# Kernel optimization log

Hardware: AMD Instinct MI355X
Metric: run time of the kernel (lower is better)

The kernel has to match this reference:

```python
import jax, jax.numpy as jnp
import numpy as np

B, H, S, D = 4, 16, 1024, 64
MAX_REL = 16  # max_relative_position


def setup_inputs() -> dict:
    key = jax.random.key(0)
    kq, kk, kv, kr = jax.random.split(key, 4)
    Q = jax.random.normal(kq, (B, H, S, D), dtype=jnp.float32)
    K = jax.random.normal(kk, (B, H, S, D), dtype=jnp.float32)
    V = jax.random.normal(kv, (B, H, S, D), dtype=jnp.float32)
    # learned relative-position embedding table [2*P+1, d_k]
    rel_table = jax.random.normal(kr, (2 * MAX_REL + 1, D), dtype=jnp.float32) * 0.02
    # causal mask, broadcastable over batch/heads; 0 => masked
    mask = jnp.tril(jnp.ones((S, S), dtype=jnp.int32))[None, None, :, :]
    return {"Q": Q, "K": K, "V": V, "rel_table": rel_table, "mask": mask}


def reference(Q, K, V, rel_table, mask):
    scale = jnp.sqrt(jnp.asarray(Q.shape[-1], Q.dtype))
    seq_len = Q.shape[2]
    r = jnp.arange(seq_len)
    # clipped relative distances -> embedding indices in [0, 2P]
    idx = jnp.clip(r[None, :] - r[:, None], -MAX_REL, MAX_REL) + MAX_REL  # [S,S]
    rel_emb = rel_table[idx]  # [S, S, D]
    scores = jnp.einsum('bhld,bhrd->bhlr', Q, K) / scale  # [B,H,S,S]
    scores = scores + jnp.einsum('bhld,lrd->bhlr', Q, rel_emb)
    scores = jnp.where(mask == 0, -jnp.inf, scores)
    attn = jax.nn.softmax(scores, axis=-1)
    output = jnp.einsum('bhlr,bhrd->bhld', attn, V)  # [B,H,S,D]
    return (output, attn)
```

## Files before the change

### kernel.cpp

```cpp
#include <hip/hip_runtime.h>

#define S_ 1024
#define D_ 64
#define RT 16
#define SCP 1036

typedef _Float16 f16x4 __attribute__((ext_vector_type(4)));
typedef _Float16 f16x8 __attribute__((ext_vector_type(8)));
typedef __fp16  h16x2 __attribute__((ext_vector_type(2)));
typedef float f32x4 __attribute__((ext_vector_type(4)));

__global__ __launch_bounds__(256)
void prep_kv(const float* __restrict__ K, const float* __restrict__ V,
             _Float16* __restrict__ Kws, _Float16* __restrict__ VT) {
    if (blockIdx.x < 1024) {
        const int idx = blockIdx.x * 256 + threadIdx.x;
        const int g4  = idx & 3;
        const float* kp = K + (size_t)(idx >> 2) * 64 + g4 * 16;
        _Float16* dst = Kws + (size_t)(idx >> 2) * 64 + g4 * 16;
        f16x8 o0, o1;
        #pragma unroll
        for (int u = 0; u < 2; ++u) {
            float4 f0 = *reinterpret_cast<const float4*>(kp + 8 * u);
            float4 f1 = *reinterpret_cast<const float4*>(kp + 8 * u + 4);
            f16x8& o = u ? o1 : o0;
            o[0] = (_Float16)f0.x; o[1] = (_Float16)f0.y;
            o[2] = (_Float16)f0.z; o[3] = (_Float16)f0.w;
            o[4] = (_Float16)f1.x; o[5] = (_Float16)f1.y;
            o[6] = (_Float16)f1.z; o[7] = (_Float16)f1.w;
        }
        *reinterpret_cast<f16x8*>(dst)     = o0;
        *reinterpret_cast<f16x8*>(dst + 8) = o1;
    } else {
        const int idx = (blockIdx.x - 1024) * 256 + threadIdx.x;
        const int bh  = idx >> 12;
        const int kt  = (idx >> 6) & 63;
        const int col = idx & 63;
        const float* vp = V + ((size_t)bh * S_ + kt * 16) * D_ + col;
        _Float16* dst = VT + ((size_t)(bh * 64 + kt) * 64 + col) * 16;
        f16x8 a, b;
        #pragma unroll
        for (int kk = 0; kk < 16; ++kk) {
            float f = vp[(size_t)kk * D_];
            if (kk < 8) a[kk] = (_Float16)f; else b[kk - 8] = (_Float16)f;
        }
        *reinterpret_cast<f16x8*>(dst)     = a;
        *reinterpret_cast<f16x8*>(dst + 8) = b;
    }
}

__global__ __launch_bounds__(256, 4)
void relattn_main(const float* __restrict__ Q, const float* __restrict__ rel,
                  const _Float16* __restrict__ Kws, const _Float16* __restrict__ VT,
                  float* __restrict__ outO, float* outA) {
    __shared__ __align__(16) _Float16 sc[RT * SCP];
    __shared__ float qrel[RT * 17];
    __shared__ float rowsum[4][RT];

    const int tid  = threadIdx.x;
    const int lane = tid & 63;
    const int w    = tid >> 6;
    const int l15  = lane & 15;
    const int g4   = lane >> 4;
    const int bid  = blockIdx.x;
    const int bh   = (bid & 7) + 8 * (bid >> 9);
    const int tile = 63 - ((bid >> 3) & 63);
    const int R0   = tile * RT;
    const int nt16 = tile + 1;

    const float* Qb = Q + (size_t)bh * S_ * D_;
    const _Float16* Kb = Kws + (size_t)bh * 64 * 1024;
    const _Float16* Vt = VT  + (size_t)bh * 64 * 1024;

    {
        const int z0 = 16 * nt16;
        const f16x8 zz = {0, 0, 0, 0, 0, 0, 0, 0};
        const int i = tid >> 4;
        for (int c = z0 + (tid & 15) * 8; c < S_; c += 128)
            *reinterpret_cast<f16x8*>(&sc[i * SCP + c]) = zz;
    }

    {
        int idx = tid;
        #pragma unroll
        for (int rep = 0; rep < 2; ++rep) {
            if (idx < RT * 17) {
                const int i = idx / 17;
                const int j = idx - i * 17;
                const float* qp = Qb + (size_t)(R0 + i) * D_;
                const float* rp = rel + j * D_;
                float s = 0.f;
                #pragma unroll
                for (int d = 0; d < D_; d += 4) {
                    float4 a = *reinterpret_cast<const float4*>(qp + d);
                    float4 b = *reinterpret_cast<const float4*>(rp + d);
                    s += a.x * b.x + a.y * b.y + a.z * b.z + a.w * b.w;
                }
                qrel[idx] = s;
            }
            idx = 256 + tid;
        }
    }

    f16x8 aq0, aq1;
    {
        const float* qp = Qb + (size_t)(R0 + l15) * D_ + 8 * g4;
        float4 f0 = *reinterpret_cast<const float4*>(qp);
        float4 f1 = *reinterpret_cast<const float4*>(qp + 4);
        float4 f2 = *reinterpret_cast<const float4*>(qp + 32);
        float4 f3 = *reinterpret_cast<const float4*>(qp + 36);
        aq0 = f16x8{(_Float16)(f0.x*0.125f), (_Float16)(f0.y*0.125f),
                    (_Float16)(f0.z*0.125f), (_Float16)(f0.w*0.125f),
                    (_Float16)(f1.x*0.125f), (_Float16)(f1.y*0.125f),
                    (_Float16)(f1.z*0.125f), (_Float16)(f1.w*0.125f)};
        aq1 = f16x8{(_Float16)(f2.x*0.125f), (_Float16)(f2.y*0.125f),
                    (_Float16)(f2.z*0.125f), (_Float16)(f2.w*0.125f),
                    (_Float16)(f3.x*0.125f), (_Float16)(f3.y*0.125f),
                    (_Float16)(f3.z*0.125f), (_Float16)(f3.w*0.125f)};
    }

    __syncthreads();

    const int   myrow = R0 + l15;
    const float qr0v  = qrel[l15 * 17];
    const int fastmax = (R0 - 31) >> 4;

    float psum = 0.f;
    auto qk_load = [&](int ct, f16x8* kf) {
        const _Float16* kp = Kb + ((size_t)ct * 16 + l15) * 64 + 8 * g4;
        kf[0] = *reinterpret_cast<const f16x8*>(kp);
        kf[1] = *reinterpret_cast<const f16x8*>(kp + 32);
    };
    auto qk_compute = [&](int ct, const f16x8* kf) {
        f32x4 acc = {0.f, 0.f, 0.f, 0.f};
        acc = __builtin_amdgcn_mfma_f32_16x16x32_f16(kf[0], aq0, acc, 0, 0, 0);
        acc = __builtin_amdgcn_mfma_f32_16x16x32_f16(kf[1], aq1, acc, 0, 0, 0);
        float e[4];
        if (ct <= fastmax) {
            #pragma unroll
            for (int j = 0; j < 4; ++j) e[j] = __expf(acc[j] + qr0v);
        } else {
            #pragma unroll
            for (int j = 0; j < 4; ++j) {
                const int dlt = myrow - (ct * 16 + 4 * g4 + j);
                e[j] = 0.f;
                if (dlt >= 0)
                    e[j] = __expf(acc[j] + ((dlt < 16) ? qrel[l15 * 17 + 16 - dlt]
                                                       : qr0v));
            }
        }
        psum += (e[0] + e[1]) + (e[2] + e[3]);
        h16x2 lo = __builtin_amdgcn_cvt_pkrtz(e[0], e[1]);
        h16x2 hi = __builtin_amdgcn_cvt_pkrtz(e[2], e[3]);
        f16x4 pk = {(_Float16)lo[0], (_Float16)lo[1],
                    (_Float16)hi[0], (_Float16)hi[1]};
        *reinterpret_cast<f16x4*>(&sc[l15 * SCP + ct * 16 + 4 * g4]) = pk;
    };

    for (int ct0 = w; ct0 < nt16; ct0 += 16) {
        f16x8 k0[2], k1[2], k2[2], k3[2];
        const bool h1 = (ct0 + 4)  < nt16;
        const bool h2 = (ct0 + 8)  < nt16;
        const bool h3 = (ct0 + 12) < nt16;
        qk_load(ct0, k0);
        if (h1) qk_load(ct0 + 4,  k1);
        if (h2) qk_load(ct0 + 8,  k2);
        if (h3) qk_load(ct0 + 12, k3);
        qk_compute(ct0, k0);
        if (h1) qk_compute(ct0 + 4,  k1);
        if (h2) qk_compute(ct0 + 8,  k2);
        if (h3) qk_compute(ct0 + 12, k3);
    }

    const int n0    = 16 * w;
    const int ktile = nt16;
    const int fg    = ktile >> 2;
    const int tail  = ktile & 3;
    const _Float16* vtb = Vt + ((size_t)(n0 + l15)) * 16 + 4 * g4;

    f16x4 bvA[4], bvB[4], bvC[4];
    auto pv_load = [&](int g, f16x4* bv) {
        #pragma unroll
        for (int u = 0; u < 4; ++u)
            bv[u] = *reinterpret_cast<const f16x4*>(vtb + (size_t)(4 * g + u) * 1024);
    };
    if (fg > 0) pv_load(0, bvA);
    if (fg > 1) pv_load(1, bvB);

    psum += __shfl_xor(psum, 16);
    psum += __shfl_xor(psum, 32);
    if (lane < 16) rowsum[w][lane] = psum;
    __syncthreads();

    f32x4 oa[4] = {{0,0,0,0},{0,0,0,0},{0,0,0,0},{0,0,0,0}};
    auto pv_mfma = [&](int g, const f16x4* bv) {
        #pragma unroll
        for (int u = 0; u < 4; ++u) {
            f16x4 ap = *reinterpret_cast<f16x4*>(
                &sc[l15 * SCP + (4 * g + u) * 16 + 4 * g4]);
            oa[u] = __builtin_amdgcn_mfma_f32_16x16x16f16(ap, bv[u], oa[u], 0, 0, 0);
        }
    };

    float* Ab = outA + ((size_t)bh * S_ + R0) * S_;
    #pragma unroll
    for (int ii = 0; ii < 4; ++ii) {
        const int i = 4 * w + ii;
        const float iv = 1.f / (rowsum[0][i] + rowsum[1][i] +
                                rowsum[2][i] + rowsum[3][i]);
        #pragma unroll
        for (int q = 0; q < 4; ++q) {
            const int c = q * 256 + lane * 4;
            f16x4 sv = *reinterpret_cast<f16x4*>(&sc[i * SCP + c]);
            f32x4 o = {(float)sv[0] * iv, (float)sv[1] * iv,
                       (float)sv[2] * iv, (float)sv[3] * iv};
            __builtin_nontemporal_store(
                o, reinterpret_cast<f32x4*>(Ab + (size_t)i * S_ + c));
        }
    }

    if (fg > 2) pv_load(2, bvC);
    int g = 0;
    for (; g + 3 < fg; g += 3) {
        pv_mfma(g, bvA);
        pv_load(g + 3, bvA);
        pv_mfma(g + 1, bvB);
        if (g + 4 < fg) pv_load(g + 4, bvB);
        pv_mfma(g + 2, bvC);
        if (g + 5 < fg) pv_load(g + 5, bvC);
    }
    if (g < fg)     pv_mfma(g, bvA);
    if (g + 1 < fg) pv_mfma(g + 1, bvB);
    if (g + 2 < fg) pv_mfma(g + 2, bvC);

    for (int r = 0; r < tail; ++r) {
        const int kt = 4 * fg + r;
        f16x4 bv = *reinterpret_cast<const f16x4*>(vtb + (size_t)kt * 1024);
        f16x4 ap = *reinterpret_cast<f16x4*>(&sc[l15 * SCP + kt * 16 + 4 * g4]);
        oa[r] = __builtin_amdgcn_mfma_f32_16x16x16f16(ap, bv, oa[r], 0, 0, 0);
    }

    f32x4 op = (oa[0] + oa[1]) + (oa[2] + oa[3]);

    float* Ob = outO + (size_t)bh * S_ * D_;
    #pragma unroll
    for (int j = 0; j < 4; ++j) {
        const int row = 4 * g4 + j;
        const float s = rowsum[0][row] + rowsum[1][row] +
                        rowsum[2][row] + rowsum[3][row];
        Ob[(size_t)(R0 + row) * D_ + n0 + l15] = op[j] / s;
    }
}

extern "C" void kernel_launch(void* const* d_in, const int* in_sizes, int n_in,
                              void* d_out, int out_size, void* d_ws, size_t ws_size,
                              hipStream_t stream) {
    const float* Q   = (const float*)d_in[0];
    const float* K   = (const float*)d_in[1];
    const float* V   = (const float*)d_in[2];
    const float* rel = (const float*)d_in[3];

    float* out  = (float*)d_out;
    float* outO = out;
    float* outA = out + (size_t)4 * 16 * 1024 * 64;

    _Float16*  Kws  = (_Float16*)((char*)d_ws + (size_t)(1 << 20));
    _Float16*  VTws = (_Float16*)((char*)d_ws + (size_t)(10 << 20));

    prep_kv<<<dim3(2048), dim3(256), 0, stream>>>(K, V, Kws, VTws);
    relattn_main<<<dim3(4096), dim3(256), 0, stream>>>(Q, rel, Kws, VTws,
                                                       outO, outA);
}
```

Before: 122.1 us.

## Double-buffer K fragment loads and trim zero-fill of score tile

The QK loop is restructured to double-buffer K fragments (kA/kB), prefetching the next group of four column tiles while computing the current one. The first K loads are issued before the block barrier so they overlap the qrel setup. The shared-memory zero fill now only covers up to the next 256-column boundary, and fully masked 256-column chunks of the attention output are written as zeros without reading shared memory. In exchange it holds 16 f16x8 buffers in registers, which may pressure occupancy under launch_bounds(256,4).

```diff
diff --git a/kernel.cpp b/kernel.cpp
--- a/kernel.cpp
+++ b/kernel.cpp
@@ -67,17 +67,18 @@
     const int tile = 63 - ((bid >> 3) & 63);
     const int R0   = tile * RT;
     const int nt16 = tile + 1;
+    const int bound = 16 * nt16;
 
     const float* Qb = Q + (size_t)bh * S_ * D_;
     const _Float16* Kb = Kws + (size_t)bh * 64 * 1024;
     const _Float16* Vt = VT  + (size_t)bh * 64 * 1024;
 
     {
-        const int z0 = 16 * nt16;
+        const int mend = (bound + 255) & ~255;
         const f16x8 zz = {0, 0, 0, 0, 0, 0, 0, 0};
-        const int i = tid >> 4;
-        for (int c = z0 + (tid & 15) * 8; c < S_; c += 128)
-            *reinterpret_cast<f16x8*>(&sc[i * SCP + c]) = zz;
+        const int r = tid >> 4;
+        for (int c = bound + (tid & 15) * 8; c < mend; c += 128)
+            *reinterpret_cast<f16x8*>(&sc[r * SCP + c]) = zz;
     }
 
     {
@@ -119,8 +120,6 @@
                     (_Float16)(f3.z*0.125f), (_Float16)(f3.w*0.125f)};
     }
 
-    __syncthreads();
-
     const int   myrow = R0 + l15;
     const float qr0v  = qrel[l15 * 17];
     const int fastmax = (R0 - 31) >> 4;
@@ -131,6 +130,20 @@
         kf[0] = *reinterpret_cast<const f16x8*>(kp);
         kf[1] = *reinterpret_cast<const f16x8*>(kp + 32);
     };
+    auto qk_load4 = [&](int ct0, f16x8* buf) {
+        #pragma unroll
+        for (int u = 0; u < 4; ++u)
+            if (ct0 + 4 * u < nt16) qk_load(ct0 + 4 * u, buf + 2 * u);
+    };
+
+    f16x8 kA[8], kB[8];
+    qk_load4(w, kA);
+
+    __syncthreads();
+
+    const float qr0 = qrel[l15 * 17];
+    (void)qr0v;
+
     auto qk_compute = [&](int ct, const f16x8* kf) {
         f32x4 acc = {0.f, 0.f, 0.f, 0.f};
         acc = __builtin_amdgcn_mfma_f32_16x16x32_f16(kf[0], aq0, acc, 0, 0, 0);
@@ -138,7 +151,7 @@
         float e[4];
         if (ct <= fastmax) {
             #pragma unroll
-            for (int j = 0; j < 4; ++j) e[j] = __expf(acc[j] + qr0v);
+            for (int j = 0; j < 4; ++j) e[j] = __expf(acc[j] + qr0);
         } else {
             #pragma unroll
             for (int j = 0; j < 4; ++j) {
@@ -146,7 +159,7 @@
                 e[j] = 0.f;
                 if (dlt >= 0)
                     e[j] = __expf(acc[j] + ((dlt < 16) ? qrel[l15 * 17 + 16 - dlt]
-                                                       : qr0v));
+                                                       : qr0));
             }
         }
         psum += (e[0] + e[1]) + (e[2] + e[3]);
@@ -156,20 +169,19 @@
                     (_Float16)hi[0], (_Float16)hi[1]};
         *reinterpret_cast<f16x4*>(&sc[l15 * SCP + ct * 16 + 4 * g4]) = pk;
     };
-
-    for (int ct0 = w; ct0 < nt16; ct0 += 16) {
-        f16x8 k0[2], k1[2], k2[2], k3[2];
-        const bool h1 = (ct0 + 4)  < nt16;
-        const bool h2 = (ct0 + 8)  < nt16;
-        const bool h3 = (ct0 + 12) < nt16;
-        qk_load(ct0, k0);
-        if (h1) qk_load(ct0 + 4,  k1);
-        if (h2) qk_load(ct0 + 8,  k2);
-        if (h3) qk_load(ct0 + 12, k3);
-        qk_compute(ct0, k0);
-        if (h1) qk_compute(ct0 + 4,  k1);
-        if (h2) qk_compute(ct0 + 8,  k2);
-        if (h3) qk_compute(ct0 + 12, k3);
+    auto qk_compute4 = [&](int ct0, const f16x8* buf) {
+        #pragma unroll
+        for (int u = 0; u < 4; ++u)
+            if (ct0 + 4 * u < nt16) qk_compute(ct0 + 4 * u, buf + 2 * u);
+    };
+
+    for (int ct0 = w; ct0 < nt16; ct0 += 32) {
+        if (ct0 + 16 < nt16) qk_load4(ct0 + 16, kB);
+        qk_compute4(ct0, kA);
+        if (ct0 + 16 < nt16) {
+            if (ct0 + 32 < nt16) qk_load4(ct0 + 32, kA);
+            qk_compute4(ct0 + 16, kB);
+        }
     }
 
     const int n0    = 16 * w;
@@ -211,9 +223,12 @@
         #pragma unroll
         for (int q = 0; q < 4; ++q) {
             const int c = q * 256 + lane * 4;
-            f16x4 sv = *reinterpret_cast<f16x4*>(&sc[i * SCP + c]);
-            f32x4 o = {(float)sv[0] * iv, (float)sv[1] * iv,
-                       (float)sv[2] * iv, (float)sv[3] * iv};
+            f32x4 o = {0.f, 0.f, 0.f, 0.f};
+            if (q * 256 < bound) {
+                f16x4 sv = *reinterpret_cast<f16x4*>(&sc[i * SCP + c]);
+                o = {(float)sv[0] * iv, (float)sv[1] * iv,
+                     (float)sv[2] * iv, (float)sv[3] * iv};
+            }
             __builtin_nontemporal_store(
                 o, reinterpret_cast<f32x4*>(Ab + (size_t)i * S_ + c));
         }
```

Measured after the change: 122.9 us. Within noise of the previous version (+0.7%).
